# Kernel optimization log

Measured on AMD Instinct MI355X. Metric: run time of the kernel, lower is better.

## Reference

```python
import jax, jax.numpy as jnp
import numpy as np

N = 100000
F = 128
H = 16
C = 40
E = 3200000


def _gcn_norm(edge_index, num_nodes):
    # add self-loops, compute symmetric normalization (PyG GCNConv default)
    loops = jnp.arange(num_nodes, dtype=edge_index.dtype)
    src = jnp.concatenate([edge_index[0], loops])
    dst = jnp.concatenate([edge_index[1], loops])
    ones = jnp.ones(src.shape[0], dtype=jnp.float32)
    deg = jax.ops.segment_sum(ones, dst, num_segments=num_nodes)
    dinv = jnp.where(deg > 0, jax.lax.rsqrt(deg), 0.0)
    norm = dinv[src] * dinv[dst]  # [E+N]
    return src, dst, norm


def _gcn_conv(x, W, b, src, dst, norm, num_nodes):
    h = x @ W                                   # [N, out] transform first (PyG order)
    msg = h[src] * norm[:, None]                # gather + scale
    agg = jax.ops.segment_sum(msg, dst, num_segments=num_nodes)  # scatter-add
    return agg + b


def setup_inputs() -> dict:
    key = jax.random.key(0)
    k = jax.random.split(key, 6)
    x = jax.random.normal(k[0], (N, F), dtype=jnp.float32)
    edge_index = jax.random.randint(k[1], (2, E), 0, N, dtype=jnp.int64)
    W1 = jax.random.normal(k[2], (F, H), dtype=jnp.float32) / np.sqrt(F)
    b1 = jnp.zeros((H,), dtype=jnp.float32)
    W2 = jax.random.normal(k[3], (H, C), dtype=jnp.float32) / np.sqrt(H)
    b2 = jnp.zeros((C,), dtype=jnp.float32)
    return {"x": x, "edge_index": edge_index, "W1": W1, "b1": b1, "W2": W2, "b2": b2}


def reference(x, edge_index, W1, b1, W2, b2):
    src, dst, norm = _gcn_norm(edge_index, N)
    h = _gcn_conv(x, W1, b1, src, dst, norm, N)
    h = jax.nn.relu(h)
    out = _gcn_conv(h, W2, b2, src, dst, norm, N)
    return out
```

## Files before the change

### kernel.cpp

```cpp
#include <hip/hip_runtime.h>
#include <hip/hip_fp16.h>


#define N_NODES 100000
#define F_IN    128
#define H_MID   16
#define C_OUT   40
#define N_EDGES 3200000

#define EC      8192
#define EBLK    391
#define NBUK    391
#define M_HIST  (NBUK * EBLK)
#define NPART   299
#define SRC_MASK 0x1FFFF
#define CAP_CSR 10240


__global__ void __launch_bounds__(1024) k_hist(
    const int* __restrict__ dst, int* __restrict__ hist) {
    __shared__ int h[NBUK];
    int t = threadIdx.x, blk = blockIdx.x;
    for (int i = t; i < NBUK; i += 1024) h[i] = 0;
    __syncthreads();
#pragma unroll
    for (int i = 0; i < EC / 1024; ++i) {
        int e = blk * EC + i * 1024 + t;
        if (e < N_EDGES) atomicAdd(&h[__builtin_nontemporal_load(dst + e) >> 8], 1);
    }
    __syncthreads();
    for (int b = t; b < NBUK; b += 1024) hist[b * EBLK + blk] = h[b];
}

__global__ void __launch_bounds__(512) k_scanA(int* __restrict__ hist,
                                               int* __restrict__ part) {
    __shared__ int s[512];
    int t = threadIdx.x;
    int i = blockIdx.x * 512 + t;
    int v = (i < M_HIST) ? hist[i] : 0;
    s[t] = v;
    __syncthreads();
    for (int off = 1; off < 512; off <<= 1) {
        int x = (t >= off) ? s[t - off] : 0;
        __syncthreads();
        s[t] += x;
        __syncthreads();
    }
    if (i < M_HIST) hist[i] = s[t] - v;
    if (t == 511) part[blockIdx.x] = s[511];
}

__global__ void __launch_bounds__(512) k_scanB(int* __restrict__ part) {
    __shared__ int s[512];
    int t = threadIdx.x;
    int v = (t < NPART) ? part[t] : 0;
    s[t] = v;
    __syncthreads();
    for (int off = 1; off < 512; off <<= 1) {
        int x = (t >= off) ? s[t - off] : 0;
        __syncthreads();
        s[t] += x;
        __syncthreads();
    }
    if (t < NPART) part[t] = s[t] - v;
}

__global__ void __launch_bounds__(1024) k_part(
    const int* __restrict__ src, const int* __restrict__ dst,
    const int* __restrict__ hist, const int* __restrict__ part,
    int* __restrict__ eb) {
    __shared__ int cnt[NBUK];
    __shared__ int scn[512];
    __shared__ int dlt[NBUK];
    __shared__ int cr[NBUK];
    __shared__ int sval[EC];
    __shared__ int spos[EC];
    int t = threadIdx.x, blk = blockIdx.x;
    for (int b = t; b < NBUK; b += 1024) cnt[b] = 0;
    __syncthreads();
    int e0 = blk * EC;
    int d[8], s[8], bk[8];
    bool val[8];
#pragma unroll
    for (int k = 0; k < 8; ++k) {
        int e = e0 + k * 1024 + t;
        val[k] = (e < N_EDGES);
        d[k] = val[k] ? __builtin_nontemporal_load(dst + e) : 0;
        s[k] = val[k] ? __builtin_nontemporal_load(src + e) : 0;
        bk[k] = d[k] >> 8;
    }
#pragma unroll
    for (int k = 0; k < 8; ++k)
        if (val[k]) atomicAdd(&cnt[bk[k]], 1);
    __syncthreads();
    if (t < 512) scn[t] = (t < NBUK) ? cnt[t] : 0;
    __syncthreads();
    for (int off = 1; off < 512; off <<= 1) {
        int x = 0;
        if (t < 512 && t >= off) x = scn[t - off];
        __syncthreads();
        if (t < 512) scn[t] += x;
        __syncthreads();
    }
    for (int b = t; b < NBUK; b += 1024) {
        int idx = b * EBLK + blk;
        int gb = hist[idx] + part[idx >> 9];
        int lb = scn[b] - cnt[b];
        dlt[b] = gb - lb;
        cr[b] = lb;
    }
    __syncthreads();
#pragma unroll
    for (int k = 0; k < 8; ++k) {
        if (val[k]) {
            int lr = atomicAdd(&cr[bk[k]], 1);
            sval[lr] = ((d[k] & 255) << 17) | s[k];
            spos[lr] = lr + dlt[bk[k]];
        }
    }
    __syncthreads();
    int n = (e0 + EC <= N_EDGES) ? EC : (N_EDGES - e0);
    for (int i = t; i < n; i += 1024)
        eb[spos[i]] = sval[i];
}

__global__ void __launch_bounds__(512) k_csr(
    const int* __restrict__ hist, const int* __restrict__ part,
    const int* __restrict__ eb,
    int* __restrict__ rp, float* __restrict__ dinv, int* __restrict__ es) {
    __shared__ int deg[256], scn[256], cw[256];
    __shared__ int esl[CAP_CSR];
    int b = blockIdx.x, t = threadIdx.x;
    int i0 = b * EBLK;
    int bb = hist[i0] + part[i0 >> 9];
    int bn = (b + 1 < NBUK) ? (hist[i0 + EBLK] + part[(i0 + EBLK) >> 9]) : N_EDGES;
    int ecnt = bn - bb;
    if (t < 256) deg[t] = 0;
    __syncthreads();
    for (int i = t; i < ecnt; i += 512)
        atomicAdd(&deg[__builtin_nontemporal_load(eb + bb + i) >> 17], 1);
    __syncthreads();
    if (t < 256) scn[t] = deg[t];
    __syncthreads();
    for (int off = 1; off < 256; off <<= 1) {
        int x = (t < 256 && t >= off) ? scn[t - off] : 0;
        __syncthreads();
        if (t < 256) scn[t] += x;
        __syncthreads();
    }
    if (t < 256) {
        int ex = scn[t] - deg[t];
        cw[t] = ex;
        int node = b * 256 + t;
        rp[node] = bb + ex;
        dinv[node] = rsqrtf(1.0f + (float)deg[t]);
    }
    __syncthreads();
    if (ecnt <= CAP_CSR) {
        for (int i = t; i < ecnt; i += 512) {
            int v = __builtin_nontemporal_load(eb + bb + i);
            int r = atomicAdd(&cw[v >> 17], 1);
            esl[r] = v & SRC_MASK;
        }
        __syncthreads();
        for (int i = t; i < ecnt; i += 512)
            __builtin_nontemporal_store(esl[i], es + bb + i);
    } else {
        for (int i = t; i < ecnt; i += 512) {
            int v = eb[bb + i];
            int r = atomicAdd(&cw[v >> 17], 1);
            es[bb + r] = v & SRC_MASK;
        }
    }
}


typedef float f4 __attribute__((ext_vector_type(4)));

__global__ void __launch_bounds__(256) k_gemm1(
    const float* __restrict__ x, const float* __restrict__ W1,
    const float* __restrict__ dinv, __half* __restrict__ h1p) {
    __shared__ float w[F_IN * H_MID];
    __shared__ float xs[16 * 132];
    int t = threadIdx.x;
    for (int i = t; i < F_IN * H_MID; i += 256) w[i] = W1[i];
    int tile = blockIdx.x;
    const f4* xg = (const f4*)(x + (size_t)tile * 16 * F_IN);
    f4* xs4 = (f4*)xs;
    for (int i = t; i < 512; i += 256) {
        int r = i >> 5, c4 = i & 31;
        xs4[r * 33 + c4] = __builtin_nontemporal_load(xg + r * 32 + c4);
    }
    __syncthreads();
    int node = t >> 4, j = t & 15;
    const float* xr = xs + node * 132;
    float acc = 0.f;
#pragma unroll 8
    for (int k = 0; k < F_IN; ++k) acc += xr[k] * w[k * H_MID + j];
    int g = tile * 16 + node;
    h1p[(size_t)g * H_MID + j] = __float2half(acc * dinv[g]);
}

__global__ void __launch_bounds__(256) k_gather1(
    const int* __restrict__ rp, const int* __restrict__ es,
    const float* __restrict__ dinv, const __half* __restrict__ h1p,
    const float* __restrict__ b1, __half* __restrict__ r1p) {
    int t = threadIdx.x;
    int node = blockIdx.x * 16 + (t >> 4), j = t & 15;
    float dv = dinv[node];
    int beg = rp[node], end = rp[node + 1];
    float acc = __half2float(h1p[(size_t)node * H_MID + j]);
    int e = beg;
    for (; e + 8 <= end; e += 8) {
        int s0 = es[e],     s1 = es[e + 1], s2 = es[e + 2], s3 = es[e + 3];
        int s4 = es[e + 4], s5 = es[e + 5], s6 = es[e + 6], s7 = es[e + 7];
        __half v0 = h1p[(size_t)s0 * H_MID + j];
        __half v1 = h1p[(size_t)s1 * H_MID + j];
        __half v2 = h1p[(size_t)s2 * H_MID + j];
        __half v3 = h1p[(size_t)s3 * H_MID + j];
        __half v4 = h1p[(size_t)s4 * H_MID + j];
        __half v5 = h1p[(size_t)s5 * H_MID + j];
        __half v6 = h1p[(size_t)s6 * H_MID + j];
        __half v7 = h1p[(size_t)s7 * H_MID + j];
        acc += __half2float(v0) + __half2float(v1) + __half2float(v2) + __half2float(v3)
             + __half2float(v4) + __half2float(v5) + __half2float(v6) + __half2float(v7);
    }
    for (; e < end; ++e) acc += __half2float(h1p[(size_t)es[e] * H_MID + j]);
    float agg1 = dv * acc;
    unsigned short o = __half_as_ushort(__float2half(fmaxf(agg1 + b1[j], 0.f) * dv));
    __builtin_nontemporal_store(o, (unsigned short*)(r1p + (size_t)node * H_MID + j));
}

__global__ void __launch_bounds__(256) k_gather2(
    const int* __restrict__ rp, const int* __restrict__ es,
    const float* __restrict__ dinv, const __half* __restrict__ r1p,
    const float* __restrict__ W2, const float* __restrict__ b2,
    float* __restrict__ out) {
    __shared__ float w2[H_MID * C_OUT];
    __shared__ float a2[16 * 17];
    int t = threadIdx.x;
    for (int i = t; i < H_MID * C_OUT; i += 256) w2[i] = W2[i];
    int tile = blockIdx.x;
    int node = tile * 16 + (t >> 4), j = t & 15;
    float dv = dinv[node];
    int beg = rp[node], end = rp[node + 1];
    float acc = __half2float(r1p[(size_t)node * H_MID + j]);
    int e = beg;
    for (; e + 8 <= end; e += 8) {
        int s0 = es[e],     s1 = es[e + 1], s2 = es[e + 2], s3 = es[e + 3];
        int s4 = es[e + 4], s5 = es[e + 5], s6 = es[e + 6], s7 = es[e + 7];
        __half v0 = r1p[(size_t)s0 * H_MID + j];
        __half v1 = r1p[(size_t)s1 * H_MID + j];
        __half v2 = r1p[(size_t)s2 * H_MID + j];
        __half v3 = r1p[(size_t)s3 * H_MID + j];
        __half v4 = r1p[(size_t)s4 * H_MID + j];
        __half v5 = r1p[(size_t)s5 * H_MID + j];
        __half v6 = r1p[(size_t)s6 * H_MID + j];
        __half v7 = r1p[(size_t)s7 * H_MID + j];
        acc += __half2float(v0) + __half2float(v1) + __half2float(v2) + __half2float(v3)
             + __half2float(v4) + __half2float(v5) + __half2float(v6) + __half2float(v7);
    }
    for (; e < end; ++e) acc += __half2float(r1p[(size_t)es[e] * H_MID + j]);
    a2[(t >> 4) * 17 + j] = dv * acc;
    __syncthreads();
    for (int idx = t; idx < 16 * C_OUT; idx += 256) {
        int nd = idx / C_OUT, c = idx % C_OUT;
        float s = b2[c];
#pragma unroll
        for (int jj = 0; jj < H_MID; ++jj) s += a2[nd * 17 + jj] * w2[jj * C_OUT + c];
        __builtin_nontemporal_store(s, &out[((size_t)tile * 16 + nd) * C_OUT + c]);
    }
}

extern "C" void kernel_launch(void* const* d_in, const int* in_sizes, int n_in,
                              void* d_out, int out_size, void* d_ws, size_t ws_size,
                              hipStream_t stream) {
    const float* x  = (const float*)d_in[0];
    const int*   ei = (const int*)d_in[1];
    const float* W1 = (const float*)d_in[2];
    const float* b1 = (const float*)d_in[3];
    const float* W2 = (const float*)d_in[4];
    const float* b2 = (const float*)d_in[5];
    float* out = (float*)d_out;

    const int* src = ei;
    const int* dst = ei + N_EDGES;

    int* rp     = (int*)d_ws;
    float* dinv = (float*)(rp + 100352);
    int* es     = (int*)(dinv + 100352);
    __half* h1p = (__half*)(es + N_EDGES);
    __half* r1p = h1p + (size_t)N_NODES * H_MID;

    int* eb   = (int*)d_out;
    int* hist = eb + N_EDGES;
    int* part = hist + 153088;

    k_hist <<<EBLK, 1024, 0, stream>>>(dst, hist);
    k_scanA<<<NPART, 512, 0, stream>>>(hist, part);
    k_scanB<<<1, 512, 0, stream>>>(part);
    k_part <<<EBLK, 1024, 0, stream>>>(src, dst, hist, part, eb);
    k_csr  <<<NBUK, 512, 0, stream>>>(hist, part, eb, rp, dinv, es);
    k_gemm1<<<N_NODES / 16, 256, 0, stream>>>(x, W1, dinv, h1p);
    k_gather1<<<N_NODES / 16, 256, 0, stream>>>(rp, es, dinv, h1p, b1, r1p);
    k_gather2<<<N_NODES / 16, 256, 0, stream>>>(rp, es, dinv, r1p, W2, b2, out);
}
```

Measured before the change: 235.3 us.

## Replace full CSR build with bucketed shared-memory atomic aggregation

```diff
diff --git a/kernel.cpp b/kernel.cpp
--- a/kernel.cpp
+++ b/kernel.cpp
@@ -14,7 +14,7 @@
 #define M_HIST  (NBUK * EBLK)
 #define NPART   299
 #define SRC_MASK 0x1FFFF
-#define CAP_CSR 10240
+#define NSTRIDE 100352
 
 
 __global__ void __launch_bounds__(1024) k_hist(
@@ -124,12 +124,10 @@
         eb[spos[i]] = sval[i];
 }
 
-__global__ void __launch_bounds__(512) k_csr(
-    const int* __restrict__ hist, const int* __restrict__ part,
-    const int* __restrict__ eb,
-    int* __restrict__ rp, float* __restrict__ dinv, int* __restrict__ es) {
-    __shared__ int deg[256], scn[256], cw[256];
-    __shared__ int esl[CAP_CSR];
+__global__ void __launch_bounds__(512) k_deg(
+    const int* __restrict__ hist, const int* __restrict__ part,
+    const int* __restrict__ eb, float* __restrict__ dinv) {
+    __shared__ int deg[256];
     int b = blockIdx.x, t = threadIdx.x;
     int i0 = b * EBLK;
     int bb = hist[i0] + part[i0 >> 9];
@@ -140,38 +138,7 @@
     for (int i = t; i < ecnt; i += 512)
         atomicAdd(&deg[__builtin_nontemporal_load(eb + bb + i) >> 17], 1);
     __syncthreads();
-    if (t < 256) scn[t] = deg[t];
-    __syncthreads();
-    for (int off = 1; off < 256; off <<= 1) {
-        int x = (t < 256 && t >= off) ? scn[t - off] : 0;
-        __syncthreads();
-        if (t < 256) scn[t] += x;
-        __syncthreads();
-    }
-    if (t < 256) {
-        int ex = scn[t] - deg[t];
-        cw[t] = ex;
-        int node = b * 256 + t;
-        rp[node] = bb + ex;
-        dinv[node] = rsqrtf(1.0f + (float)deg[t]);
-    }
-    __syncthreads();
-    if (ecnt <= CAP_CSR) {
-        for (int i = t; i < ecnt; i += 512) {
-            int v = __builtin_nontemporal_load(eb + bb + i);
-            int r = atomicAdd(&cw[v >> 17], 1);
-            esl[r] = v & SRC_MASK;
-        }
-        __syncthreads();
-        for (int i = t; i < ecnt; i += 512)
-            __builtin_nontemporal_store(esl[i], es + bb + i);
-    } else {
-        for (int i = t; i < ecnt; i += 512) {
-            int v = eb[bb + i];
-            int r = atomicAdd(&cw[v >> 17], 1);
-            es[bb + r] = v & SRC_MASK;
-        }
-    }
+    if (t < 256) dinv[b * 256 + t] = rsqrtf(1.0f + (float)deg[t]);
 }
 
 
@@ -201,74 +168,93 @@
     h1p[(size_t)g * H_MID + j] = __float2half(acc * dinv[g]);
 }
 
-__global__ void __launch_bounds__(256) k_gather1(
-    const int* __restrict__ rp, const int* __restrict__ es,
-    const float* __restrict__ dinv, const __half* __restrict__ h1p,
-    const float* __restrict__ b1, __half* __restrict__ r1p) {
-    int t = threadIdx.x;
-    int node = blockIdx.x * 16 + (t >> 4), j = t & 15;
-    float dv = dinv[node];
-    int beg = rp[node], end = rp[node + 1];
-    float acc = __half2float(h1p[(size_t)node * H_MID + j]);
-    int e = beg;
-    for (; e + 8 <= end; e += 8) {
-        int s0 = es[e],     s1 = es[e + 1], s2 = es[e + 2], s3 = es[e + 3];
-        int s4 = es[e + 4], s5 = es[e + 5], s6 = es[e + 6], s7 = es[e + 7];
-        __half v0 = h1p[(size_t)s0 * H_MID + j];
-        __half v1 = h1p[(size_t)s1 * H_MID + j];
-        __half v2 = h1p[(size_t)s2 * H_MID + j];
-        __half v3 = h1p[(size_t)s3 * H_MID + j];
-        __half v4 = h1p[(size_t)s4 * H_MID + j];
-        __half v5 = h1p[(size_t)s5 * H_MID + j];
-        __half v6 = h1p[(size_t)s6 * H_MID + j];
-        __half v7 = h1p[(size_t)s7 * H_MID + j];
-        acc += __half2float(v0) + __half2float(v1) + __half2float(v2) + __half2float(v3)
-             + __half2float(v4) + __half2float(v5) + __half2float(v6) + __half2float(v7);
-    }
-    for (; e < end; ++e) acc += __half2float(h1p[(size_t)es[e] * H_MID + j]);
-    float agg1 = dv * acc;
-    unsigned short o = __half_as_ushort(__float2half(fmaxf(agg1 + b1[j], 0.f) * dv));
-    __builtin_nontemporal_store(o, (unsigned short*)(r1p + (size_t)node * H_MID + j));
-}
-
-__global__ void __launch_bounds__(256) k_gather2(
-    const int* __restrict__ rp, const int* __restrict__ es,
-    const float* __restrict__ dinv, const __half* __restrict__ r1p,
-    const float* __restrict__ W2, const float* __restrict__ b2,
-    float* __restrict__ out) {
+__global__ void __launch_bounds__(1024) k_agg1(
+    const int* __restrict__ hist, const int* __restrict__ part,
+    const int* __restrict__ eb, const float* __restrict__ dinv,
+    const __half* __restrict__ h1p, const float* __restrict__ b1,
+    __half* __restrict__ r1p) {
+    __shared__ float acc[256 * H_MID];
+    int b = blockIdx.x, t = threadIdx.x;
+    int i0 = b * EBLK;
+    int bb = hist[i0] + part[i0 >> 9];
+    int bn = (b + 1 < NBUK) ? (hist[i0 + EBLK] + part[(i0 + EBLK) >> 9]) : N_EDGES;
+    int ecnt = bn - bb;
+    for (int i = t; i < 256 * H_MID; i += 1024)
+        acc[i] = __half2float(h1p[(size_t)b * 4096 + i]);
+    __syncthreads();
+    int g = t >> 4, j = t & 15;
+    for (int base = 0; base < ecnt; base += 256) {
+        int v[4];
+        float hv[4];
+#pragma unroll
+        for (int k = 0; k < 4; ++k) {
+            int ii = base + (k << 6) + g;
+            v[k] = (ii < ecnt) ? __builtin_nontemporal_load(eb + bb + ii) : -1;
+        }
+#pragma unroll
+        for (int k = 0; k < 4; ++k)
+            if (v[k] >= 0) hv[k] = __half2float(h1p[(size_t)(v[k] & SRC_MASK) * H_MID + j]);
+#pragma unroll
+        for (int k = 0; k < 4; ++k)
+            if (v[k] >= 0) atomicAdd(&acc[((v[k] >> 17) << 4) + j], hv[k]);
+    }
+    __syncthreads();
+    for (int i = t; i < 256 * H_MID; i += 1024) {
+        int node = b * 256 + (i >> 4);
+        float dv = dinv[node];
+        float a = dv * acc[i];
+        unsigned short o = __half_as_ushort(__float2half(fmaxf(a + b1[i & 15], 0.f) * dv));
+        __builtin_nontemporal_store(o, (unsigned short*)(r1p + (size_t)b * 4096 + i));
+    }
+}
+
+__global__ void __launch_bounds__(1024) k_agg2(
+    const int* __restrict__ hist, const int* __restrict__ part,
+    const int* __restrict__ eb, const float* __restrict__ dinv,
+    const __half* __restrict__ r1p, const float* __restrict__ W2,
+    const float* __restrict__ b2, float* __restrict__ out) {
+    __shared__ float acc[256 * H_MID];
     __shared__ float w2[H_MID * C_OUT];
-    __shared__ float a2[16 * 17];
-    int t = threadIdx.x;
-    for (int i = t; i < H_MID * C_OUT; i += 256) w2[i] = W2[i];
-    int tile = blockIdx.x;
-    int node = tile * 16 + (t >> 4), j = t & 15;
-    float dv = dinv[node];
-    int beg = rp[node], end = rp[node + 1];
-    float acc = __half2float(r1p[(size_t)node * H_MID + j]);
-    int e = beg;
-    for (; e + 8 <= end; e += 8) {
-        int s0 = es[e],     s1 = es[e + 1], s2 = es[e + 2], s3 = es[e + 3];
-        int s4 = es[e + 4], s5 = es[e + 5], s6 = es[e + 6], s7 = es[e + 7];
-        __half v0 = r1p[(size_t)s0 * H_MID + j];
-        __half v1 = r1p[(size_t)s1 * H_MID + j];
-        __half v2 = r1p[(size_t)s2 * H_MID + j];
-        __half v3 = r1p[(size_t)s3 * H_MID + j];
-        __half v4 = r1p[(size_t)s4 * H_MID + j];
-        __half v5 = r1p[(size_t)s5 * H_MID + j];
-        __half v6 = r1p[(size_t)s6 * H_MID + j];
-        __half v7 = r1p[(size_t)s7 * H_MID + j];
-        acc += __half2float(v0) + __half2float(v1) + __half2float(v2) + __half2float(v3)
-             + __half2float(v4) + __half2float(v5) + __half2float(v6) + __half2float(v7);
-    }
-    for (; e < end; ++e) acc += __half2float(r1p[(size_t)es[e] * H_MID + j]);
-    a2[(t >> 4) * 17 + j] = dv * acc;
-    __syncthreads();
-    for (int idx = t; idx < 16 * C_OUT; idx += 256) {
-        int nd = idx / C_OUT, c = idx % C_OUT;
-        float s = b2[c];
-#pragma unroll
-        for (int jj = 0; jj < H_MID; ++jj) s += a2[nd * 17 + jj] * w2[jj * C_OUT + c];
-        __builtin_nontemporal_store(s, &out[((size_t)tile * 16 + nd) * C_OUT + c]);
+    __shared__ float b2l[C_OUT];
+    int b = blockIdx.x, t = threadIdx.x;
+    int i0 = b * EBLK;
+    int bb = hist[i0] + part[i0 >> 9];
+    int bn = (b + 1 < NBUK) ? (hist[i0 + EBLK] + part[(i0 + EBLK) >> 9]) : N_EDGES;
+    int ecnt = bn - bb;
+    for (int i = t; i < H_MID * C_OUT; i += 1024) w2[i] = W2[i];
+    if (t < C_OUT) b2l[t] = b2[t];
+    for (int i = t; i < 256 * H_MID; i += 1024)
+        acc[i] = __half2float(r1p[(size_t)b * 4096 + i]);
+    __syncthreads();
+    int g = t >> 4, j = t & 15;
+    for (int base = 0; base < ecnt; base += 256) {
+        int v[4];
+        float hv[4];
+#pragma unroll
+        for (int k = 0; k < 4; ++k) {
+            int ii = base + (k << 6) + g;
+            v[k] = (ii < ecnt) ? __builtin_nontemporal_load(eb + bb + ii) : -1;
+        }
+#pragma unroll
+        for (int k = 0; k < 4; ++k)
+            if (v[k] >= 0) hv[k] = __half2float(r1p[(size_t)(v[k] & SRC_MASK) * H_MID + j]);
+#pragma unroll
+        for (int k = 0; k < 4; ++k)
+            if (v[k] >= 0) atomicAdd(&acc[((v[k] >> 17) << 4) + j], hv[k]);
+    }
+    __syncthreads();
+    for (int i = t; i < 256 * H_MID; i += 1024)
+        acc[i] *= dinv[b * 256 + (i >> 4)];
+    __syncthreads();
+    for (int idx = t; idx < 256 * C_OUT; idx += 1024) {
+        int nd = idx / C_OUT, c = idx - nd * C_OUT;
+        int node = b * 256 + nd;
+        if (node < N_NODES) {
+            float s = b2l[c];
+#pragma unroll
+            for (int jj = 0; jj < H_MID; ++jj) s += acc[nd * H_MID + jj] * w2[jj * C_OUT + c];
+            __builtin_nontemporal_store(s, &out[(size_t)node * C_OUT + c]);
+        }
     }
 }
 
@@ -286,22 +272,19 @@
     const int* src = ei;
     const int* dst = ei + N_EDGES;
 
-    int* rp     = (int*)d_ws;
-    float* dinv = (float*)(rp + 100352);
-    int* es     = (int*)(dinv + 100352);
-    __half* h1p = (__half*)(es + N_EDGES);
-    __half* r1p = h1p + (size_t)N_NODES * H_MID;
-
-    int* eb   = (int*)d_out;
-    int* hist = eb + N_EDGES;
-    int* part = hist + 153088;
+    float* dinv = (float*)d_ws;
+    __half* h1p = (__half*)(dinv + NSTRIDE);
+    __half* r1p = h1p + (size_t)NSTRIDE * H_MID;
+    int* eb     = (int*)(r1p + (size_t)NSTRIDE * H_MID);
+    int* hist   = eb + N_EDGES;
+    int* part   = hist + 153088;
 
     k_hist <<<EBLK, 1024, 0, stream>>>(dst, hist);
     k_scanA<<<NPART, 512, 0, stream>>>(hist, part);
     k_scanB<<<1, 512, 0, stream>>>(part);
     k_part <<<EBLK, 1024, 0, stream>>>(src, dst, hist, part, eb);
-    k_csr  <<<NBUK, 512, 0, stream>>>(hist, part, eb, rp, dinv, es);
+    k_deg  <<<NBUK, 512, 0, stream>>>(hist, part, eb, dinv);
     k_gemm1<<<N_NODES / 16, 256, 0, stream>>>(x, W1, dinv, h1p);
-    k_gather1<<<N_NODES / 16, 256, 0, stream>>>(rp, es, dinv, h1p, b1, r1p);
-    k_gather2<<<N_NODES / 16, 256, 0, stream>>>(rp, es, dinv, r1p, W2, b2, out);
-}
+    k_agg1 <<<NBUK, 1024, 0, stream>>>(hist, part, eb, dinv, h1p, b1, r1p);
+    k_agg2 <<<NBUK, 1024, 0, stream>>>(hist, part, eb, dinv, r1p, W2, b2, out);
+}
```

New measurement: 849.9 us. 3.61x slower.

## Fuse CSR source scatter into first-layer gather using shared-memory edge lists

Applied to the files above, without the earlier changes.

```diff
diff --git a/kernel.cpp b/kernel.cpp
--- a/kernel.cpp
+++ b/kernel.cpp
@@ -14,7 +14,8 @@
 #define M_HIST  (NBUK * EBLK)
 #define NPART   299
 #define SRC_MASK 0x1FFFF
-#define CAP_CSR 10240
+#define NSTRIDE 100352
+#define CAP_H   5632
 
 
 __global__ void __launch_bounds__(1024) k_hist(
@@ -124,12 +125,11 @@
         eb[spos[i]] = sval[i];
 }
 
-__global__ void __launch_bounds__(512) k_csr(
+__global__ void __launch_bounds__(512) k_degrp(
     const int* __restrict__ hist, const int* __restrict__ part,
-    const int* __restrict__ eb,
-    int* __restrict__ rp, float* __restrict__ dinv, int* __restrict__ es) {
-    __shared__ int deg[256], scn[256], cw[256];
-    __shared__ int esl[CAP_CSR];
+    const int* __restrict__ eb, int* __restrict__ rp,
+    float* __restrict__ dinv) {
+    __shared__ int deg[256], scn[256];
     int b = blockIdx.x, t = threadIdx.x;
     int i0 = b * EBLK;
     int bb = hist[i0] + part[i0 >> 9];
@@ -150,27 +150,9 @@
     }
     if (t < 256) {
         int ex = scn[t] - deg[t];
-        cw[t] = ex;
         int node = b * 256 + t;
         rp[node] = bb + ex;
         dinv[node] = rsqrtf(1.0f + (float)deg[t]);
-    }
-    __syncthreads();
-    if (ecnt <= CAP_CSR) {
-        for (int i = t; i < ecnt; i += 512) {
-            int v = __builtin_nontemporal_load(eb + bb + i);
-            int r = atomicAdd(&cw[v >> 17], 1);
-            esl[r] = v & SRC_MASK;
-        }
-        __syncthreads();
-        for (int i = t; i < ecnt; i += 512)
-            __builtin_nontemporal_store(esl[i], es + bb + i);
-    } else {
-        for (int i = t; i < ecnt; i += 512) {
-            int v = eb[bb + i];
-            int r = atomicAdd(&cw[v >> 17], 1);
-            es[bb + r] = v & SRC_MASK;
-        }
     }
 }
 
@@ -201,34 +183,93 @@
     h1p[(size_t)g * H_MID + j] = __float2half(acc * dinv[g]);
 }
 
-__global__ void __launch_bounds__(256) k_gather1(
-    const int* __restrict__ rp, const int* __restrict__ es,
+__global__ void __launch_bounds__(1024) k_csrg1(
+    const int* __restrict__ hist, const int* __restrict__ part,
+    const int* __restrict__ eb, const int* __restrict__ rp,
     const float* __restrict__ dinv, const __half* __restrict__ h1p,
-    const float* __restrict__ b1, __half* __restrict__ r1p) {
-    int t = threadIdx.x;
-    int node = blockIdx.x * 16 + (t >> 4), j = t & 15;
-    float dv = dinv[node];
-    int beg = rp[node], end = rp[node + 1];
-    float acc = __half2float(h1p[(size_t)node * H_MID + j]);
-    int e = beg;
-    for (; e + 8 <= end; e += 8) {
-        int s0 = es[e],     s1 = es[e + 1], s2 = es[e + 2], s3 = es[e + 3];
-        int s4 = es[e + 4], s5 = es[e + 5], s6 = es[e + 6], s7 = es[e + 7];
-        __half v0 = h1p[(size_t)s0 * H_MID + j];
-        __half v1 = h1p[(size_t)s1 * H_MID + j];
-        __half v2 = h1p[(size_t)s2 * H_MID + j];
-        __half v3 = h1p[(size_t)s3 * H_MID + j];
-        __half v4 = h1p[(size_t)s4 * H_MID + j];
-        __half v5 = h1p[(size_t)s5 * H_MID + j];
-        __half v6 = h1p[(size_t)s6 * H_MID + j];
-        __half v7 = h1p[(size_t)s7 * H_MID + j];
-        acc += __half2float(v0) + __half2float(v1) + __half2float(v2) + __half2float(v3)
-             + __half2float(v4) + __half2float(v5) + __half2float(v6) + __half2float(v7);
-    }
-    for (; e < end; ++e) acc += __half2float(h1p[(size_t)es[e] * H_MID + j]);
-    float agg1 = dv * acc;
-    unsigned short o = __half_as_ushort(__float2half(fmaxf(agg1 + b1[j], 0.f) * dv));
-    __builtin_nontemporal_store(o, (unsigned short*)(r1p + (size_t)node * H_MID + j));
+    const float* __restrict__ b1, int* __restrict__ es,
+    __half* __restrict__ r1p) {
+    __shared__ int base[129];
+    __shared__ int cw[128];
+    __shared__ int esl[CAP_H];
+    int bh = blockIdx.x;
+    int b = bh >> 1, hi = bh & 1;
+    int t = threadIdx.x;
+    int i0 = b * EBLK;
+    int bb = hist[i0] + part[i0 >> 9];
+    int bn = (b + 1 < NBUK) ? (hist[i0 + EBLK] + part[(i0 + EBLK) >> 9]) : N_EDGES;
+    int ecnt = bn - bb;
+    int n0 = b * 256 + hi * 128;
+    if (t < 128) {
+        int lb = rp[n0 + t] - bb;
+        base[t] = lb;
+        cw[t] = lb;
+    }
+    if (t == 128) base[128] = hi ? ecnt : (rp[b * 256 + 128] - bb);
+    __syncthreads();
+    int h0 = base[0];
+    int hcnt = base[128] - h0;
+    int g = t >> 4, j = t & 15;
+    if (hcnt <= CAP_H) {
+        for (int i = t; i < ecnt; i += 1024) {
+            int v = __builtin_nontemporal_load(eb + bb + i);
+            int loc = v >> 17;
+            if ((loc >> 7) == hi) {
+                int r = atomicAdd(&cw[loc & 127], 1);
+                esl[r - h0] = v & SRC_MASK;
+            }
+        }
+        __syncthreads();
+        for (int i = t; i < hcnt; i += 1024)
+            __builtin_nontemporal_store(esl[i], es + bb + h0 + i);
+        for (int nd = g; nd < 128; nd += 64) {
+            int node = n0 + nd;
+            if (node >= N_NODES) continue;
+            float dv = dinv[node];
+            int beg = base[nd] - h0, end = base[nd + 1] - h0;
+            float acc = __half2float(h1p[(size_t)node * H_MID + j]);
+            int e = beg;
+            for (; e + 8 <= end; e += 8) {
+                int s0 = esl[e],     s1 = esl[e + 1], s2 = esl[e + 2], s3 = esl[e + 3];
+                int s4 = esl[e + 4], s5 = esl[e + 5], s6 = esl[e + 6], s7 = esl[e + 7];
+                acc += __half2float(h1p[(size_t)s0 * H_MID + j])
+                     + __half2float(h1p[(size_t)s1 * H_MID + j])
+                     + __half2float(h1p[(size_t)s2 * H_MID + j])
+                     + __half2float(h1p[(size_t)s3 * H_MID + j])
+                     + __half2float(h1p[(size_t)s4 * H_MID + j])
+                     + __half2float(h1p[(size_t)s5 * H_MID + j])
+                     + __half2float(h1p[(size_t)s6 * H_MID + j])
+                     + __half2float(h1p[(size_t)s7 * H_MID + j]);
+            }
+            for (; e < end; ++e) acc += __half2float(h1p[(size_t)esl[e] * H_MID + j]);
+            float a = dv * acc;
+            unsigned short o = __half_as_ushort(__float2half(fmaxf(a + b1[j], 0.f) * dv));
+            __builtin_nontemporal_store(o, (unsigned short*)(r1p + (size_t)node * H_MID + j));
+        }
+    } else {
+        for (int i = t; i < ecnt; i += 1024) {
+            int v = eb[bb + i];
+            int loc = v >> 17;
+            if ((loc >> 7) == hi) {
+                int r = atomicAdd(&cw[loc & 127], 1);
+                es[bb + r] = v & SRC_MASK;
+            }
+        }
+        __threadfence_block();
+        __syncthreads();
+        for (int nd = g; nd < 128; nd += 64) {
+            int node = n0 + nd;
+            if (node >= N_NODES) continue;
+            float dv = dinv[node];
+            int beg = bb + base[nd], end = bb + base[nd + 1];
+            float acc = __half2float(h1p[(size_t)node * H_MID + j]);
+            for (int e = beg; e < end; ++e)
+                acc += __half2float(h1p[(size_t)es[e] * H_MID + j]);
+            float a = dv * acc;
+            unsigned short o = __half_as_ushort(__float2half(fmaxf(a + b1[j], 0.f) * dv));
+            __builtin_nontemporal_store(o, (unsigned short*)(r1p + (size_t)node * H_MID + j));
+        }
+    }
 }
 
 __global__ void __launch_bounds__(256) k_gather2(
@@ -249,22 +290,20 @@
     for (; e + 8 <= end; e += 8) {
         int s0 = es[e],     s1 = es[e + 1], s2 = es[e + 2], s3 = es[e + 3];
         int s4 = es[e + 4], s5 = es[e + 5], s6 = es[e + 6], s7 = es[e + 7];
-        __half v0 = r1p[(size_t)s0 * H_MID + j];
-        __half v1 = r1p[(size_t)s1 * H_MID + j];
-        __half v2 = r1p[(size_t)s2 * H_MID + j];
-        __half v3 = r1p[(size_t)s3 * H_MID + j];
-        __half v4 = r1p[(size_t)s4 * H_MID + j];
-        __half v5 = r1p[(size_t)s5 * H_MID + j];
-        __half v6 = r1p[(size_t)s6 * H_MID + j];
-        __half v7 = r1p[(size_t)s7 * H_MID + j];
-        acc += __half2float(v0) + __half2float(v1) + __half2float(v2) + __half2float(v3)
-             + __half2float(v4) + __half2float(v5) + __half2float(v6) + __half2float(v7);
+        acc += __half2float(r1p[(size_t)s0 * H_MID + j])
+             + __half2float(r1p[(size_t)s1 * H_MID + j])
+             + __half2float(r1p[(size_t)s2 * H_MID + j])
+             + __half2float(r1p[(size_t)s3 * H_MID + j])
+             + __half2float(r1p[(size_t)s4 * H_MID + j])
+             + __half2float(r1p[(size_t)s5 * H_MID + j])
+             + __half2float(r1p[(size_t)s6 * H_MID + j])
+             + __half2float(r1p[(size_t)s7 * H_MID + j]);
     }
     for (; e < end; ++e) acc += __half2float(r1p[(size_t)es[e] * H_MID + j]);
     a2[(t >> 4) * 17 + j] = dv * acc;
     __syncthreads();
     for (int idx = t; idx < 16 * C_OUT; idx += 256) {
-        int nd = idx / C_OUT, c = idx % C_OUT;
+        int nd = idx / C_OUT, c = idx - nd * C_OUT;
         float s = b2[c];
 #pragma unroll
         for (int jj = 0; jj < H_MID; ++jj) s += a2[nd * 17 + jj] * w2[jj * C_OUT + c];
@@ -287,10 +326,10 @@
     const int* dst = ei + N_EDGES;
 
     int* rp     = (int*)d_ws;
-    float* dinv = (float*)(rp + 100352);
-    int* es     = (int*)(dinv + 100352);
+    float* dinv = (float*)(rp + NSTRIDE);
+    int* es     = (int*)(dinv + NSTRIDE);
     __half* h1p = (__half*)(es + N_EDGES);
-    __half* r1p = h1p + (size_t)N_NODES * H_MID;
+    __half* r1p = h1p + (size_t)NSTRIDE * H_MID;
 
     int* eb   = (int*)d_out;
     int* hist = eb + N_EDGES;
@@ -300,8 +339,8 @@
     k_scanA<<<NPART, 512, 0, stream>>>(hist, part);
     k_scanB<<<1, 512, 0, stream>>>(part);
     k_part <<<EBLK, 1024, 0, stream>>>(src, dst, hist, part, eb);
-    k_csr  <<<NBUK, 512, 0, stream>>>(hist, part, eb, rp, dinv, es);
+    k_degrp<<<NBUK, 512, 0, stream>>>(hist, part, eb, rp, dinv);
     k_gemm1<<<N_NODES / 16, 256, 0, stream>>>(x, W1, dinv, h1p);
-    k_gather1<<<N_NODES / 16, 256, 0, stream>>>(rp, es, dinv, h1p, b1, r1p);
+    k_csrg1<<<NBUK * 2, 1024, 0, stream>>>(hist, part, eb, rp, dinv, h1p, b1, es, r1p);
     k_gather2<<<N_NODES / 16, 256, 0, stream>>>(rp, es, dinv, r1p, W2, b2, out);
 }
```

Result: no change. 236.7 us (+0.6%).
